# Optimization experiments

Hardware: AMD Instinct MI355X
Metric: run time of the kernel (lower is better)

## Reference

```python
import jax, jax.numpy as jnp
import numpy as np
import math

C = 512          # channels
K = 3            # conv kernel size
DILATIONS = (1, 3, 5)
RATIO = 2        # up/down sample ratio
FK = 12          # FIR anti-alias kernel size


def kaiser_sinc_filter1d(cutoff, half_width, kernel_size):
    # BigVGAN alias-free kaiser-windowed sinc lowpass filter
    half_size = kernel_size // 2
    delta_f = 4.0 * half_width
    A = 2.285 * (half_size - 1) * math.pi * delta_f + 7.95
    if A > 50.0:
        beta = 0.1102 * (A - 8.7)
    elif A >= 21.0:
        beta = 0.5842 * (A - 21.0) ** 0.4 + 0.07886 * (A - 21.0)
    else:
        beta = 0.0
    window = np.kaiser(kernel_size, beta)
    if kernel_size % 2 == 0:
        time = np.arange(-half_size, half_size) + 0.5
    else:
        time = np.arange(kernel_size) - half_size
    filt = 2.0 * cutoff * window * np.sinc(2.0 * cutoff * time)
    filt = filt / filt.sum()
    return jnp.asarray(filt, dtype=jnp.float32)

# Up/Down both use cutoff=0.5/ratio, half_width=0.6/ratio, kernel=12
AA_FILTER = kaiser_sinc_filter1d(0.5 / RATIO, 0.6 / RATIO, FK)

UP_PAD = FK // RATIO - 1                               # 5 (replicate pad before transpose conv)
UP_PAD_LEFT = UP_PAD * RATIO + (FK - RATIO) // 2       # 15
UP_PAD_RIGHT = UP_PAD * RATIO + (FK - RATIO + 1) // 2  # 15
DN_PAD_LEFT = FK // 2 - 1                              # 5 (even kernel)
DN_PAD_RIGHT = FK // 2                                 # 6


def _depthwise_conv(x, filt, stride=1, lhs_dilation=1, padding=(0, 0)):
    c = x.shape[1]
    w = jnp.broadcast_to(filt.reshape(1, 1, -1), (c, 1, filt.shape[0]))
    return jax.lax.conv_general_dilated(
        x, w, window_strides=(stride,), padding=[padding],
        lhs_dilation=(lhs_dilation,), dimension_numbers=('NCH', 'OIH', 'NCH'),
        feature_group_count=c)


def upsample2x(x):
    # replicate pad, depthwise transposed conv (lhs-dilated conv w/ flipped kernel), crop, scale
    x = jnp.pad(x, ((0, 0), (0, 0), (UP_PAD, UP_PAD)), mode='edge')
    y = RATIO * _depthwise_conv(x, AA_FILTER[::-1], lhs_dilation=RATIO,
                                padding=(FK - 1, FK - 1))
    return y[..., UP_PAD_LEFT:-UP_PAD_RIGHT]


def downsample2x(x):
    x = jnp.pad(x, ((0, 0), (0, 0), (DN_PAD_LEFT, DN_PAD_RIGHT)), mode='edge')
    return _depthwise_conv(x, AA_FILTER, stride=RATIO)


def snake_log(x, alpha, beta):
    # use_log_scale=True: alpha/beta are exponentiated; x + 1/(b+1e-5) * sin(a*x)^2
    a = jnp.exp(alpha)[None, :, None]
    b = jnp.exp(beta)[None, :, None]
    return x + (1.0 / (b + 1e-5)) * jnp.square(jnp.sin(x * a))


def aliasing_activation(x, alpha, beta):
    return downsample2x(snake_log(upsample2x(x), alpha, beta))


def weight_norm_conv1d(x, v, g, bias, dilation):
    # torch weight_norm dim=0: W[o] = g[o] * v[o] / ||v[o]||
    norm = jnp.sqrt(jnp.sum(v * v, axis=(1, 2), keepdims=True))
    w = g[:, None, None] * v / norm
    pad = (K * dilation - dilation) // 2
    y = jax.lax.conv_general_dilated(
        x, w, window_strides=(1,), padding=[(pad, pad)],
        rhs_dilation=(dilation,), dimension_numbers=('NCH', 'OIH', 'NCH'))
    return y + bias[None, :, None]


def setup_inputs() -> dict:
    key = jax.random.key(0)
    ks = jax.random.split(key, 12)
    B, T = 16, 4096
    return {
        'x': jax.random.normal(ks[0], (B, C, T), dtype=jnp.float32),
        'float_masks': jnp.ones((B, 1, T), dtype=jnp.float32),
        'in_snake_alpha': 0.1 * jax.random.normal(ks[1], (3, C), dtype=jnp.float32),
        'in_snake_beta': 0.1 * jax.random.normal(ks[2], (3, C), dtype=jnp.float32),
        'out_snake_alpha': 0.1 * jax.random.normal(ks[3], (3, C), dtype=jnp.float32),
        'out_snake_beta': 0.1 * jax.random.normal(ks[4], (3, C), dtype=jnp.float32),
        'in_conv_v': 0.05 * jax.random.normal(ks[5], (3, C, C, K), dtype=jnp.float32),
        'in_conv_g': 1.0 + 0.01 * jax.random.normal(ks[6], (3, C), dtype=jnp.float32),
        'in_conv_b': 0.01 * jax.random.normal(ks[7], (3, C), dtype=jnp.float32),
        'out_conv_v': 0.05 * jax.random.normal(ks[8], (3, C, C, K), dtype=jnp.float32),
        'out_conv_g': 1.0 + 0.01 * jax.random.normal(ks[9], (3, C), dtype=jnp.float32),
        'out_conv_b': 0.01 * jax.random.normal(ks[10], (3, C), dtype=jnp.float32),
    }


def reference(x, float_masks, in_snake_alpha, in_snake_beta, out_snake_alpha,
              out_snake_beta, in_conv_v, in_conv_g, in_conv_b, out_conv_v,
              out_conv_g, out_conv_b):
    for i, dilation in enumerate(DILATIONS):
        residuals = x
        x = aliasing_activation(x, in_snake_alpha[i], in_snake_beta[i]) * float_masks
        x = weight_norm_conv1d(x, in_conv_v[i], in_conv_g[i], in_conv_b[i], dilation)
        x = aliasing_activation(x, out_snake_alpha[i], out_snake_beta[i]) * float_masks
        x = weight_norm_conv1d(x, out_conv_v[i], out_conv_g[i], out_conv_b[i], 1)
        x = x + residuals
    return x * float_masks
```

## Files before the change

kernel.cpp:

```cpp
#include <hip/hip_runtime.h>
#include <cmath>

#define BN_ 16
#define CN_ 512
#define TN_ 4096
#define TPAD_ 4112
#define PADR_ 8

typedef float f32x4 __attribute__((ext_vector_type(4)));
typedef __bf16 bf16x8 __attribute__((ext_vector_type(8)));
typedef unsigned short u16x8 __attribute__((ext_vector_type(8)));

struct AAFilt { float g0[6]; float g1[6]; float fE[6]; float fO[6]; };

__device__ __forceinline__ unsigned short f2bf(float f) {
  unsigned u = __builtin_bit_cast(unsigned, f);
  u = (u + 0x7fffu + ((u >> 16) & 1u)) >> 16;
  return (unsigned short)u;
}
__device__ __forceinline__ float bf2f(unsigned short h) {
  return __builtin_bit_cast(float, (unsigned)h << 16);
}
__device__ __forceinline__ float to_f(float x) { return x; }
__device__ __forceinline__ float to_f(unsigned short x) { return bf2f(x); }

__device__ __forceinline__ void gld16(const void* g, void* l) {
  __builtin_amdgcn_global_load_lds((const __attribute__((address_space(1))) void*)g,
                                   (__attribute__((address_space(3))) void*)l,
                                   16, 0, 0);
}

__global__ __launch_bounds__(256) void prep_w(
    const float* __restrict__ vin, const float* __restrict__ gin,
    const float* __restrict__ vout, const float* __restrict__ gout,
    unsigned short* __restrict__ wpack)
{
  const int o = blockIdx.x;
  const int l = blockIdx.y;
  const int i = l >> 1, oc = l & 1;
  const float* v = (oc ? vout : vin) + (size_t)i * CN_ * CN_ * 3 + (size_t)o * CN_ * 3;
  const float g = (oc ? gout : gin)[i * CN_ + o];
  const int tid = threadIdx.x;

  float a = 0.f;
  for (int j = tid; j < 1536; j += 256) { float x = v[j]; a += x * x; }
  #pragma unroll
  for (int off = 32; off > 0; off >>= 1) a += __shfl_down(a, off);
  __shared__ float red[4];
  if ((tid & 63) == 0) red[tid >> 6] = a;
  __syncthreads();
  const float tot = red[0] + red[1] + red[2] + red[3];
  const float scale = g / sqrtf(tot);
  unsigned short* wl = wpack + (size_t)l * 3 * CN_ * CN_;
  for (int j = tid; j < 1536; j += 256) {
    int c = j / 3, k = j - 3 * c;
    wl[((size_t)k * CN_ + o) * CN_ + c] = f2bf(v[j] * scale);
  }
}

__global__ __launch_bounds__(256) void transpose_in(
    const float* __restrict__ src, float* __restrict__ dst)
{
  __shared__ float tile[32][33];
  const int b = blockIdx.z, c0 = blockIdx.y * 32, t0 = blockIdx.x * 32;
  const int tx = threadIdx.x & 31, ty = threadIdx.x >> 5;
  const float* s = src + ((size_t)b * CN_ + c0) * TN_ + t0;
  #pragma unroll
  for (int j = 0; j < 32; j += 8) tile[ty + j][tx] = s[(size_t)(ty + j) * TN_ + tx];
  __syncthreads();
  float* d = dst + ((size_t)b * TN_ + t0) * CN_ + c0;
  #pragma unroll
  for (int j = 0; j < 32; j += 8) d[(size_t)(ty + j) * CN_ + tx] = tile[tx][ty + j];
}

template <typename TIN>
__global__ __launch_bounds__(512) void act_kernel(
    const TIN* __restrict__ src, unsigned short* __restrict__ dst,
    const float* __restrict__ alpha, const float* __restrict__ beta,
    const float* __restrict__ mask, AAFilt F)
{
  const int c = threadIdx.x;
  const int b = blockIdx.y;
  const int seg = blockIdx.x;
  const int t0 = seg << 7;
  const float av = expf(alpha[c]);
  const float ib = 1.0f / (expf(beta[c]) + 1e-5f);
  const TIN* row = src + (size_t)b * TN_ * CN_ + c;
  unsigned short* drow = dst + (size_t)b * TPAD_ * CN_ + c;
  const float* mrow = mask + (size_t)b * TN_;

  if (seg == 0)  { for (int p = 0; p < PADR_; ++p) drow[(size_t)p * CN_] = 0; }
  if (seg == 31) { for (int p = 0; p < PADR_; ++p) drow[(size_t)(TPAD_ - PADR_ + p) * CN_] = 0; }

  auto ldx = [&](int t) -> float {
    t = t < 0 ? 0 : (t > TN_ - 1 ? TN_ - 1 : t);
    return to_f(row[(size_t)t * CN_]);
  };

  float xw[6];
  #pragma unroll
  for (int j = 0; j < 6; ++j) xw[j] = ldx(t0 - 5 + j);
  float sE[6], sO[6];
  #pragma unroll
  for (int j = 0; j < 6; ++j) { sE[j] = 0.f; sO[j] = 0.f; }
  float s_last = 0.f;

  auto step = [&](int tau, bool emit) {
    float uO = 0.f, uE = 0.f;
    #pragma unroll
    for (int j = 0; j < 6; ++j) { uO += F.g1[j] * xw[j]; uE += F.g0[j] * xw[j]; }
    float so = __sinf(uO * av); float sOn = uO + ib * so * so;
    float se = __sinf(uE * av); float sEn = uE + ib * se * se;
    if (tau + 2 == TN_ - 1) s_last = sOn;
    if (tau + 2 >= TN_) sOn = s_last;
    if (tau + 3 >= TN_) sEn = s_last;
    #pragma unroll
    for (int j = 0; j < 5; ++j) { sE[j] = sE[j + 1]; sO[j] = sO[j + 1]; }
    sE[5] = sEn; sO[5] = sOn;
    if (emit) {
      float d = 0.f;
      #pragma unroll
      for (int j = 0; j < 6; ++j) d += F.fE[j] * sE[j] + F.fO[j] * sO[j];
      d *= mrow[tau];
      drow[(size_t)(PADR_ + tau) * CN_] = f2bf(d);
    }
    #pragma unroll
    for (int j = 0; j < 5; ++j) xw[j] = xw[j + 1];
    xw[5] = ldx(tau + 6);
  };

  for (int w = 0; w < 5; ++w) step(t0 - 5 + w, false);
  if (t0 == 0) {
    float s0 = sE[3];
    sE[1] = s0; sE[2] = s0;
    sO[1] = s0; sO[2] = s0; sO[3] = s0;
  }
  for (int t = t0; t < t0 + 128; ++t) step(t, true);
}

#define ASZ (272 * 32)
#define BSZ (3 * 256 * 32)

template <int MODE>
__global__ __launch_bounds__(512, 2) void conv_kernel(
    const unsigned short* __restrict__ act,
    const unsigned short* __restrict__ wp,
    const float* __restrict__ bias,
    const float* __restrict__ res,
    const float* __restrict__ mask,
    void* __restrict__ outp, int dil)
{
  __shared__ __align__(16) unsigned short lA[2 * ASZ];
  __shared__ __align__(16) unsigned short lB[2 * BSZ];

  const int tid = threadIdx.x;
  const int bid = blockIdx.x;
  const int xcd = bid & 7, j = bid >> 3;
  const int ob = j & 1, tile = j >> 1;
  const int tt = tile * 8 + xcd;
  const int b = tt >> 4;
  const int t0 = (tt & 15) << 8;
  const int o0 = ob << 8;

  const int lane = tid & 63;
  const int wave = tid >> 6;
  const int wm = wave >> 2, wn = wave & 3;

  const f32x4 zero = {0.f, 0.f, 0.f, 0.f};
  f32x4 acc[8][4];
  #pragma unroll
  for (int a = 0; a < 8; ++a)
    #pragma unroll
    for (int n = 0; n < 4; ++n) acc[a][n] = zero;

  const unsigned short* aBase = act + ((size_t)b * TPAD_ + t0) * CN_;

  auto stage = [&](int bufi, int cb) {
    const int c0 = cb * 32;
    unsigned short* A = lA + (size_t)bufi * ASZ;
    unsigned short* B = lB + (size_t)bufi * BSZ;
    #pragma unroll
    for (int it = 0; it < 2; ++it) {
      int p = tid + it * 512;
      int r = p >> 2, pq = p & 3, gq = pq ^ (r & 3);
      gld16(aBase + (size_t)r * CN_ + c0 + gq * 8, A + (size_t)p * 8);
    }
    if (tid < 64) {
      int p = tid + 1024;
      int r = p >> 2, pq = p & 3, gq = pq ^ (r & 3);
      gld16(aBase + (size_t)r * CN_ + c0 + gq * 8, A + (size_t)p * 8);
    }
    #pragma unroll
    for (int it = 0; it < 6; ++it) {
      int p = tid + it * 512;
      int k = p >> 10, rem = p & 1023, ol = rem >> 2, pq = rem & 3;
      int gq = pq ^ (ol & 3);
      gld16(wp + ((size_t)(k * CN_ + o0 + ol)) * CN_ + c0 + gq * 8, B + (size_t)p * 8);
    }
  };

  stage(0, 0);
  __syncthreads();

  for (int cb = 0; cb < 16; ++cb) {
    const int cur = cb & 1;
    if (cb < 15) stage(cur ^ 1, cb + 1);
    const unsigned short* A = lA + (size_t)cur * ASZ;
    const unsigned short* B = lB + (size_t)cur * BSZ;

    #pragma unroll
    for (int k = 0; k < 3; ++k) {
      bf16x8 af[8], bfr[4];
      #pragma unroll
      for (int mi = 0; mi < 8; ++mi) {
        int r = wm * 128 + (lane & 15) + mi * 16 + PADR_ + (k - 1) * dil;
        int q = (lane >> 4) ^ (r & 3);
        af[mi] = __builtin_bit_cast(bf16x8, *reinterpret_cast<const u16x8*>(A + ((size_t)r * 4 + q) * 8));
      }
      #pragma unroll
      for (int ni = 0; ni < 4; ++ni) {
        int ol = wn * 64 + ni * 16 + (lane & 15);
        int q = (lane >> 4) ^ (ol & 3);
        bfr[ni] = __builtin_bit_cast(bf16x8, *reinterpret_cast<const u16x8*>(B + (((size_t)k * 256 + ol) * 4 + q) * 8));
      }
      __builtin_amdgcn_s_setprio(1);
      #pragma unroll
      for (int mi = 0; mi < 8; ++mi)
        #pragma unroll
        for (int ni = 0; ni < 4; ++ni)
          acc[mi][ni] = __builtin_amdgcn_mfma_f32_16x16x32_bf16(af[mi], bfr[ni], acc[mi][ni], 0, 0, 0);
      __builtin_amdgcn_s_setprio(0);
    }
    __syncthreads();
  }

  const int olane = lane & 15, rg = lane >> 4;
  const int obase = o0 + wn * 64 + olane;
  const int tbase = t0 + wm * 128 + rg * 4;

  if (MODE == 0) {
    unsigned short* O = (unsigned short*)outp + (size_t)b * TN_ * CN_;
    #pragma unroll
    for (int ni = 0; ni < 4; ++ni) {
      float bv = bias[obase + ni * 16];
      #pragma unroll
      for (int mi = 0; mi < 8; ++mi) {
        #pragma unroll
        for (int r = 0; r < 4; ++r) {
          int t = tbase + mi * 16 + r;
          O[(size_t)t * CN_ + obase + ni * 16] = f2bf(acc[mi][ni][r] + bv);
        }
      }
    }
  } else if (MODE == 1) {
    float* O = (float*)outp + (size_t)b * TN_ * CN_;
    const float* R = res + (size_t)b * TN_ * CN_;
    #pragma unroll
    for (int ni = 0; ni < 4; ++ni) {
      float bv = bias[obase + ni * 16];
      #pragma unroll
      for (int mi = 0; mi < 8; ++mi) {
        #pragma unroll
        for (int r = 0; r < 4; ++r) {
          int t = tbase + mi * 16 + r;
          size_t ix = (size_t)t * CN_ + obase + ni * 16;
          O[ix] = acc[mi][ni][r] + bv + R[ix];
        }
      }
    }
  } else {
    float* O = (float*)outp + (size_t)b * CN_ * TN_;
    const float* R = res + (size_t)b * TN_ * CN_;
    const float* M = mask + (size_t)b * TN_;
    float bv[4];
    #pragma unroll
    for (int ni = 0; ni < 4; ++ni) bv[ni] = bias[obase + ni * 16];
    #pragma unroll
    for (int mi = 0; mi < 8; ++mi) {
      int t = tbase + mi * 16;
      f32x4 mv = *reinterpret_cast<const f32x4*>(M + t);
      #pragma unroll
      for (int ni = 0; ni < 4; ++ni) {
        f32x4 v;
        #pragma unroll
        for (int r = 0; r < 4; ++r)
          v[r] = (acc[mi][ni][r] + bv[ni] + R[(size_t)(t + r) * CN_ + obase + ni * 16]) * mv[r];
        *reinterpret_cast<f32x4*>(O + (size_t)(obase + ni * 16) * TN_ + t) = v;
      }
    }
  }
}

static double bi0(double x) {
  double s = 1.0, t = 1.0, q = x * x * 0.25;
  for (int k = 1; k < 50; ++k) { t *= q / ((double)k * (double)k); s += t; if (t < 1e-18 * s) break; }
  return s;
}
static void make_filt(AAFilt* F) {
  const double PI = 3.14159265358979323846;
  double A = 2.285 * 5.0 * PI * 1.2 + 7.95;
  double beta;
  if (A > 50.0) beta = 0.1102 * (A - 8.7);
  else if (A >= 21.0) beta = 0.5842 * pow(A - 21.0, 0.4) + 0.07886 * (A - 21.0);
  else beta = 0.0;
  double i0b = bi0(beta);
  double f[12], sum = 0.0;
  for (int n = 0; n < 12; ++n) {
    double xx = 2.0 * n / 11.0 - 1.0;
    double w = bi0(beta * sqrt(fmax(0.0, 1.0 - xx * xx))) / i0b;
    double tt = (double)(n - 6) + 0.5;
    double arg = 0.5 * tt;
    double snc = sin(PI * arg) / (PI * arg);
    f[n] = 0.5 * w * snc;
    sum += f[n];
  }
  for (int n = 0; n < 12; ++n) f[n] /= sum;
  for (int j = 0; j < 6; ++j) {
    F->g0[j] = (float)(2.0 * f[11 - 2 * j]);
    F->g1[j] = (float)(2.0 * f[10 - 2 * j]);
    F->fE[j] = (float)f[2 * j + 1];
    F->fO[j] = (float)f[2 * j];
  }
}

extern "C" void kernel_launch(void* const* d_in, const int* in_sizes, int n_in,
                              void* d_out, int out_size, void* d_ws, size_t ws_size,
                              hipStream_t stream)
{
  (void)in_sizes; (void)n_in; (void)out_size; (void)ws_size;
  const float* x    = (const float*)d_in[0];
  const float* mask = (const float*)d_in[1];
  const float* inA  = (const float*)d_in[2];
  const float* inB  = (const float*)d_in[3];
  const float* outA = (const float*)d_in[4];
  const float* outB = (const float*)d_in[5];
  const float* vin  = (const float*)d_in[6];
  const float* gin  = (const float*)d_in[7];
  const float* bin  = (const float*)d_in[8];
  const float* vout = (const float*)d_in[9];
  const float* gout = (const float*)d_in[10];
  const float* bout = (const float*)d_in[11];

  char* ws = (char*)d_ws;
  float* xta           = (float*)ws;
  unsigned short* actb = (unsigned short*)(ws + 134217728);
  unsigned short* y1   = (unsigned short*)(ws + 134217728 + 67371008);
  unsigned short* wpk  = (unsigned short*)(ws + 134217728 + 67371008 + 67108864);

  AAFilt F; make_filt(&F);

  prep_w<<<dim3(512, 6), dim3(256), 0, stream>>>(vin, gin, vout, gout, wpk);
  transpose_in<<<dim3(128, 16, 16), dim3(256), 0, stream>>>(x, xta);

  const int dils[3] = {1, 3, 5};
  float* xcur = xta;
  float* dof = (float*)d_out;
  for (int i = 0; i < 3; ++i) {
    act_kernel<float><<<dim3(32, 16), dim3(512), 0, stream>>>(
        xcur, actb, inA + i * CN_, inB + i * CN_, mask, F);
    conv_kernel<0><<<dim3(512), dim3(512), 0, stream>>>(
        actb, wpk + (size_t)(2 * i) * 3 * CN_ * CN_, bin + i * CN_,
        nullptr, mask, (void*)y1, dils[i]);
    act_kernel<unsigned short><<<dim3(32, 16), dim3(512), 0, stream>>>(
        y1, actb, outA + i * CN_, outB + i * CN_, mask, F);
    if (i < 2) {
      float* xnext = (i == 0) ? dof : xta;
      conv_kernel<1><<<dim3(512), dim3(512), 0, stream>>>(
          actb, wpk + (size_t)(2 * i + 1) * 3 * CN_ * CN_, bout + i * CN_,
          xcur, mask, (void*)xnext, 1);
      xcur = xnext;
    } else {
      conv_kernel<2><<<dim3(512), dim3(512), 0, stream>>>(
          actb, wpk + (size_t)(2 * i + 1) * 3 * CN_ * CN_, bout + i * CN_,
          xcur, mask, d_out, 1);
    }
  }
}
```

Before: 1.253 ms.

## Interleave global prefetch with MFMA phases using fine-grained waitcnt and barriers

Restructures the conv GEMM main loop into six sub-phases per channel block. Each phase reads half of the A fragments plus the B fragments for one tap, issues part of the next block's global-to-LDS loads, and runs 16 MFMAs under raised priority. Explicit vmcnt and lgkmcnt waits replace whole-block __syncthreads, and the LDS swizzle changes from r&3 to (r>>1)&3. The goal is to overlap memory traffic with compute, reduce bank conflicts and cut register pressure from the A fragments. In exchange it adds many more barriers, and the hand-counted vmcnt values are fragile.

```diff
diff --git a/kernel.cpp b/kernel.cpp
--- a/kernel.cpp
+++ b/kernel.cpp
@@ -141,6 +141,43 @@
 #define ASZ (272 * 32)
 #define BSZ (3 * 256 * 32)
 
+#define VMCNT(n) asm volatile("s_waitcnt vmcnt(" #n ")" ::: "memory")
+#define LGKMCNT0 do { asm volatile("s_waitcnt lgkmcnt(0)" ::: "memory"); \
+                      __builtin_amdgcn_sched_barrier(0); } while (0)
+#define BAR __builtin_amdgcn_s_barrier()
+#define PRIO1 __builtin_amdgcn_s_setprio(1)
+#define PRIO0 __builtin_amdgcn_s_setprio(0)
+
+#define READ_A(k, mlo) do { \
+    const int rb_ = rbase[k] + (mlo) * 16; \
+    const int q_ = q4 ^ ((rb_ >> 1) & 3); \
+    const unsigned short* ap_ = A + ((size_t)rb_ * 4 + q_) * 8; \
+    af[0] = __builtin_bit_cast(bf16x8, *(const u16x8*)(ap_)); \
+    af[1] = __builtin_bit_cast(bf16x8, *(const u16x8*)(ap_ + 512)); \
+    af[2] = __builtin_bit_cast(bf16x8, *(const u16x8*)(ap_ + 1024)); \
+    af[3] = __builtin_bit_cast(bf16x8, *(const u16x8*)(ap_ + 1536)); \
+  } while (0)
+
+#define READ_B(k) do { \
+    const int ob_ = wn * 64 + l15; \
+    const int q_ = q4 ^ ((ob_ >> 1) & 3); \
+    const unsigned short* bp_ = Bc + (((size_t)(k) * 256 + ob_) * 4 + q_) * 8; \
+    bfr[0] = __builtin_bit_cast(bf16x8, *(const u16x8*)(bp_)); \
+    bfr[1] = __builtin_bit_cast(bf16x8, *(const u16x8*)(bp_ + 512)); \
+    bfr[2] = __builtin_bit_cast(bf16x8, *(const u16x8*)(bp_ + 1024)); \
+    bfr[3] = __builtin_bit_cast(bf16x8, *(const u16x8*)(bp_ + 1536)); \
+  } while (0)
+
+#define MFMA16(mlo) do { \
+    _Pragma("unroll") \
+    for (int mi_ = 0; mi_ < 4; ++mi_) { \
+      _Pragma("unroll") \
+      for (int ni_ = 0; ni_ < 4; ++ni_) \
+        acc[(mlo) + mi_][ni_] = __builtin_amdgcn_mfma_f32_16x16x32_bf16( \
+            af[mi_], bfr[ni_], acc[(mlo) + mi_][ni_], 0, 0, 0); \
+    } \
+  } while (0)
+
 template <int MODE>
 __global__ __launch_bounds__(512, 2) void conv_kernel(
     const unsigned short* __restrict__ act,
@@ -165,6 +202,7 @@
   const int lane = tid & 63;
   const int wave = tid >> 6;
   const int wm = wave >> 2, wn = wave & 3;
+  const int l15 = lane & 15, q4 = lane >> 4;
 
   const f32x4 zero = {0.f, 0.f, 0.f, 0.f};
   f32x4 acc[8][4];
@@ -175,68 +213,72 @@
 
   const unsigned short* aBase = act + ((size_t)b * TPAD_ + t0) * CN_;
 
-  auto stage = [&](int bufi, int cb) {
-    const int c0 = cb * 32;
-    unsigned short* A = lA + (size_t)bufi * ASZ;
-    unsigned short* B = lB + (size_t)bufi * BSZ;
-    #pragma unroll
-    for (int it = 0; it < 2; ++it) {
-      int p = tid + it * 512;
-      int r = p >> 2, pq = p & 3, gq = pq ^ (r & 3);
-      gld16(aBase + (size_t)r * CN_ + c0 + gq * 8, A + (size_t)p * 8);
-    }
+  int rbase[3];
+  #pragma unroll
+  for (int k = 0; k < 3; ++k) rbase[k] = wm * 128 + l15 + PADR_ + (k - 1) * dil;
+
+  auto stageA = [&](unsigned short* Ad, int c0) {
+    { int p = tid;       int r = p >> 2, pq = p & 3, gq = pq ^ ((r >> 1) & 3);
+      gld16(aBase + (size_t)r * CN_ + c0 + gq * 8, Ad + (size_t)p * 8); }
+    { int p = tid + 512; int r = p >> 2, pq = p & 3, gq = pq ^ ((r >> 1) & 3);
+      gld16(aBase + (size_t)r * CN_ + c0 + gq * 8, Ad + (size_t)p * 8); }
     if (tid < 64) {
-      int p = tid + 1024;
-      int r = p >> 2, pq = p & 3, gq = pq ^ (r & 3);
-      gld16(aBase + (size_t)r * CN_ + c0 + gq * 8, A + (size_t)p * 8);
-    }
-    #pragma unroll
-    for (int it = 0; it < 6; ++it) {
-      int p = tid + it * 512;
-      int k = p >> 10, rem = p & 1023, ol = rem >> 2, pq = rem & 3;
-      int gq = pq ^ (ol & 3);
-      gld16(wp + ((size_t)(k * CN_ + o0 + ol)) * CN_ + c0 + gq * 8, B + (size_t)p * 8);
-    }
+      int p = tid + 1024; int r = p >> 2, pq = p & 3, gq = pq ^ ((r >> 1) & 3);
+      gld16(aBase + (size_t)r * CN_ + c0 + gq * 8, Ad + (size_t)p * 8); }
   };
-
-  stage(0, 0);
-  __syncthreads();
-
-  for (int cb = 0; cb < 16; ++cb) {
-    const int cur = cb & 1;
-    if (cb < 15) stage(cur ^ 1, cb + 1);
-    const unsigned short* A = lA + (size_t)cur * ASZ;
-    const unsigned short* B = lB + (size_t)cur * BSZ;
-
-    #pragma unroll
-    for (int k = 0; k < 3; ++k) {
-      bf16x8 af[8], bfr[4];
-      #pragma unroll
-      for (int mi = 0; mi < 8; ++mi) {
-        int r = wm * 128 + (lane & 15) + mi * 16 + PADR_ + (k - 1) * dil;
-        int q = (lane >> 4) ^ (r & 3);
-        af[mi] = __builtin_bit_cast(bf16x8, *reinterpret_cast<const u16x8*>(A + ((size_t)r * 4 + q) * 8));
-      }
-      #pragma unroll
-      for (int ni = 0; ni < 4; ++ni) {
-        int ol = wn * 64 + ni * 16 + (lane & 15);
-        int q = (lane >> 4) ^ (ol & 3);
-        bfr[ni] = __builtin_bit_cast(bf16x8, *reinterpret_cast<const u16x8*>(B + (((size_t)k * 256 + ol) * 4 + q) * 8));
-      }
-      __builtin_amdgcn_s_setprio(1);
-      #pragma unroll
-      for (int mi = 0; mi < 8; ++mi)
-        #pragma unroll
-        for (int ni = 0; ni < 4; ++ni)
-          acc[mi][ni] = __builtin_amdgcn_mfma_f32_16x16x32_bf16(af[mi], bfr[ni], acc[mi][ni], 0, 0, 0);
-      __builtin_amdgcn_s_setprio(0);
-    }
-    __syncthreads();
-  }
-
-  const int olane = lane & 15, rg = lane >> 4;
-  const int obase = o0 + wn * 64 + olane;
-  const int tbase = t0 + wm * 128 + rg * 4;
+  auto stageB = [&](unsigned short* Bd, int c0, int k) {
+    { int p = tid;       int ol = p >> 2, pq = p & 3, gq = pq ^ ((ol >> 1) & 3);
+      gld16(wp + ((size_t)(k * CN_) + o0 + ol) * CN_ + c0 + gq * 8,
+            Bd + ((size_t)k * 1024 + p) * 8); }
+    { int p = tid + 512; int ol = p >> 2, pq = p & 3, gq = pq ^ ((ol >> 1) & 3);
+      gld16(wp + ((size_t)(k * CN_) + o0 + ol) * CN_ + c0 + gq * 8,
+            Bd + ((size_t)k * 1024 + p) * 8); }
+  };
+
+  stageA(lA, 0); stageB(lB, 0, 0); stageB(lB, 0, 1); stageB(lB, 0, 2);
+  VMCNT(4);
+  BAR;
+
+  for (int cb = 0; cb < 15; ++cb) {
+    const unsigned short* A  = lA + (size_t)(cb & 1) * ASZ;
+    const unsigned short* Bc = lB + (size_t)(cb & 1) * BSZ;
+    unsigned short* An = lA + (size_t)((cb & 1) ^ 1) * ASZ;
+    unsigned short* Bn = lB + (size_t)((cb & 1) ^ 1) * BSZ;
+    const int c0n = (cb + 1) * 32;
+    bf16x8 af[4], bfr[4];
+    READ_A(0, 0); READ_B(0); stageA(An, c0n);
+    BAR; LGKMCNT0; PRIO1; MFMA16(0); PRIO0; BAR;
+    READ_A(0, 4); stageB(Bn, c0n, 0);
+    BAR; LGKMCNT0; PRIO1; MFMA16(4); PRIO0; VMCNT(6); BAR;
+    READ_A(1, 0); READ_B(1); stageB(Bn, c0n, 1);
+    BAR; LGKMCNT0; PRIO1; MFMA16(0); PRIO0; BAR;
+    READ_A(1, 4); stageB(Bn, c0n, 2);
+    BAR; LGKMCNT0; PRIO1; MFMA16(4); PRIO0; VMCNT(6); BAR;
+    READ_A(2, 0); READ_B(2);
+    BAR; LGKMCNT0; PRIO1; MFMA16(0); PRIO0; BAR;
+    READ_A(2, 4);
+    BAR; LGKMCNT0; PRIO1; MFMA16(4); PRIO0; VMCNT(4); BAR;
+  }
+  {
+    const unsigned short* A  = lA + ASZ;
+    const unsigned short* Bc = lB + BSZ;
+    bf16x8 af[4], bfr[4];
+    READ_A(0, 0); READ_B(0);
+    BAR; LGKMCNT0; PRIO1; MFMA16(0); PRIO0; BAR;
+    READ_A(0, 4);
+    BAR; LGKMCNT0; PRIO1; MFMA16(4); PRIO0; VMCNT(2); BAR;
+    READ_A(1, 0); READ_B(1);
+    BAR; LGKMCNT0; PRIO1; MFMA16(0); PRIO0; BAR;
+    READ_A(1, 4);
+    BAR; LGKMCNT0; PRIO1; MFMA16(4); PRIO0; VMCNT(0); BAR;
+    READ_A(2, 0); READ_B(2);
+    BAR; LGKMCNT0; PRIO1; MFMA16(0); PRIO0; BAR;
+    READ_A(2, 4);
+    BAR; LGKMCNT0; PRIO1; MFMA16(4); PRIO0;
+  }
+
+  const int obase = o0 + wn * 64 + l15;
+  const int tbase = t0 + wm * 128 + q4 * 4;
 
   if (MODE == 0) {
     unsigned short* O = (unsigned short*)outp + (size_t)b * TN_ * CN_;
```

After: 1.187 ms. 5.3% less time.

## Loop output-channel halves per block, template dilation, and change LDS swizzle

Applied to the files above, without the earlier changes.

Each conv block now computes both 256-wide output-channel halves sequentially instead of launching separate blocks, halving the grid to 256 blocks. Dilation becomes a compile-time template parameter so row offsets fold into constants. The LDS XOR swizzle uses (row>>1)&3 to change the bank-conflict pattern, and s_setprio hints and the trailing barrier are removed. Halving the grid risks leaving compute units underused at two blocks per CU.

```diff
diff --git a/kernel.cpp b/kernel.cpp
--- a/kernel.cpp
+++ b/kernel.cpp
@@ -141,151 +141,153 @@
 #define ASZ (272 * 32)
 #define BSZ (3 * 256 * 32)
 
-template <int MODE>
+template <int MODE, int DIL>
 __global__ __launch_bounds__(512, 2) void conv_kernel(
     const unsigned short* __restrict__ act,
     const unsigned short* __restrict__ wp,
     const float* __restrict__ bias,
     const float* __restrict__ res,
     const float* __restrict__ mask,
-    void* __restrict__ outp, int dil)
+    void* __restrict__ outp)
 {
   __shared__ __align__(16) unsigned short lA[2 * ASZ];
   __shared__ __align__(16) unsigned short lB[2 * BSZ];
 
   const int tid = threadIdx.x;
   const int bid = blockIdx.x;
-  const int xcd = bid & 7, j = bid >> 3;
-  const int ob = j & 1, tile = j >> 1;
-  const int tt = tile * 8 + xcd;
+  const int xcd = bid & 7, grp = bid >> 3;
+  const int tt = grp * 8 + xcd;
   const int b = tt >> 4;
   const int t0 = (tt & 15) << 8;
-  const int o0 = ob << 8;
 
   const int lane = tid & 63;
   const int wave = tid >> 6;
   const int wm = wave >> 2, wn = wave & 3;
-
-  const f32x4 zero = {0.f, 0.f, 0.f, 0.f};
-  f32x4 acc[8][4];
-  #pragma unroll
-  for (int a = 0; a < 8; ++a)
-    #pragma unroll
-    for (int n = 0; n < 4; ++n) acc[a][n] = zero;
+  const int l15 = lane & 15, q4 = lane >> 4;
 
   const unsigned short* aBase = act + ((size_t)b * TPAD_ + t0) * CN_;
 
-  auto stage = [&](int bufi, int cb) {
+  auto stage = [&](int bufi, int cb, int o0) {
     const int c0 = cb * 32;
-    unsigned short* A = lA + (size_t)bufi * ASZ;
-    unsigned short* B = lB + (size_t)bufi * BSZ;
-    #pragma unroll
-    for (int it = 0; it < 2; ++it) {
-      int p = tid + it * 512;
-      int r = p >> 2, pq = p & 3, gq = pq ^ (r & 3);
-      gld16(aBase + (size_t)r * CN_ + c0 + gq * 8, A + (size_t)p * 8);
-    }
+    unsigned short* Ad = lA + (size_t)bufi * ASZ;
+    unsigned short* Bd = lB + (size_t)bufi * BSZ;
+    { int p = tid;       int r = p >> 2, pq = p & 3, gq = pq ^ ((r >> 1) & 3);
+      gld16(aBase + (size_t)r * CN_ + c0 + gq * 8, Ad + (size_t)p * 8); }
+    { int p = tid + 512; int r = p >> 2, pq = p & 3, gq = pq ^ ((r >> 1) & 3);
+      gld16(aBase + (size_t)r * CN_ + c0 + gq * 8, Ad + (size_t)p * 8); }
     if (tid < 64) {
       int p = tid + 1024;
-      int r = p >> 2, pq = p & 3, gq = pq ^ (r & 3);
-      gld16(aBase + (size_t)r * CN_ + c0 + gq * 8, A + (size_t)p * 8);
+      int r = p >> 2, pq = p & 3, gq = pq ^ ((r >> 1) & 3);
+      gld16(aBase + (size_t)r * CN_ + c0 + gq * 8, Ad + (size_t)p * 8);
     }
     #pragma unroll
     for (int it = 0; it < 6; ++it) {
       int p = tid + it * 512;
       int k = p >> 10, rem = p & 1023, ol = rem >> 2, pq = rem & 3;
-      int gq = pq ^ (ol & 3);
-      gld16(wp + ((size_t)(k * CN_ + o0 + ol)) * CN_ + c0 + gq * 8, B + (size_t)p * 8);
+      int gq = pq ^ ((ol >> 1) & 3);
+      gld16(wp + ((size_t)(k * CN_) + o0 + ol) * CN_ + c0 + gq * 8,
+            Bd + (size_t)p * 8);
     }
   };
 
-  stage(0, 0);
-  __syncthreads();
-
-  for (int cb = 0; cb < 16; ++cb) {
-    const int cur = cb & 1;
-    if (cb < 15) stage(cur ^ 1, cb + 1);
-    const unsigned short* A = lA + (size_t)cur * ASZ;
-    const unsigned short* B = lB + (size_t)cur * BSZ;
-
-    #pragma unroll
-    for (int k = 0; k < 3; ++k) {
-      bf16x8 af[8], bfr[4];
+  for (int h = 0; h < 2; ++h) {
+    const int o0 = h << 8;
+
+    const f32x4 zero = {0.f, 0.f, 0.f, 0.f};
+    f32x4 acc[8][4];
+    #pragma unroll
+    for (int a = 0; a < 8; ++a)
+      #pragma unroll
+      for (int n = 0; n < 4; ++n) acc[a][n] = zero;
+
+    stage(0, 0, o0);
+    __syncthreads();
+
+    for (int cb = 0; cb < 16; ++cb) {
+      const unsigned short* A  = lA + (size_t)(cb & 1) * ASZ;
+      const unsigned short* Bc = lB + (size_t)(cb & 1) * BSZ;
+      if (cb < 15) stage((cb & 1) ^ 1, cb + 1, o0);
+
+      #pragma unroll
+      for (int k = 0; k < 3; ++k) {
+        bf16x8 af[8], bfr[4];
+        const int rb0 = wm * 128 + l15 + PADR_ + (k - 1) * DIL;
+        #pragma unroll
+        for (int mi = 0; mi < 8; ++mi) {
+          int r = rb0 + mi * 16;
+          int q = q4 ^ ((r >> 1) & 3);
+          af[mi] = __builtin_bit_cast(bf16x8,
+                     *reinterpret_cast<const u16x8*>(A + ((size_t)r * 4 + q) * 8));
+        }
+        #pragma unroll
+        for (int ni = 0; ni < 4; ++ni) {
+          int ol = wn * 64 + ni * 16 + l15;
+          int q = q4 ^ ((ol >> 1) & 3);
+          bfr[ni] = __builtin_bit_cast(bf16x8,
+                      *reinterpret_cast<const u16x8*>(Bc + (((size_t)k * 256 + ol) * 4 + q) * 8));
+        }
+        #pragma unroll
+        for (int mi = 0; mi < 8; ++mi)
+          #pragma unroll
+          for (int ni = 0; ni < 4; ++ni)
+            acc[mi][ni] = __builtin_amdgcn_mfma_f32_16x16x32_bf16(
+                af[mi], bfr[ni], acc[mi][ni], 0, 0, 0);
+      }
+      if (cb < 15) __syncthreads();
+    }
+
+    const int obase = o0 + wn * 64 + l15;
+    const int tbase = t0 + wm * 128 + q4 * 4;
+
+    if (MODE == 0) {
+      unsigned short* O = (unsigned short*)outp + (size_t)b * TN_ * CN_;
+      #pragma unroll
+      for (int ni = 0; ni < 4; ++ni) {
+        float bv = bias[obase + ni * 16];
+        #pragma unroll
+        for (int mi = 0; mi < 8; ++mi) {
+          #pragma unroll
+          for (int r = 0; r < 4; ++r) {
+            int t = tbase + mi * 16 + r;
+            O[(size_t)t * CN_ + obase + ni * 16] = f2bf(acc[mi][ni][r] + bv);
+          }
+        }
+      }
+    } else if (MODE == 1) {
+      float* O = (float*)outp + (size_t)b * TN_ * CN_;
+      const float* R = res + (size_t)b * TN_ * CN_;
+      #pragma unroll
+      for (int ni = 0; ni < 4; ++ni) {
+        float bv = bias[obase + ni * 16];
+        #pragma unroll
+        for (int mi = 0; mi < 8; ++mi) {
+          #pragma unroll
+          for (int r = 0; r < 4; ++r) {
+            int t = tbase + mi * 16 + r;
+            size_t ix = (size_t)t * CN_ + obase + ni * 16;
+            O[ix] = acc[mi][ni][r] + bv + R[ix];
+          }
+        }
+      }
+    } else {
+      float* O = (float*)outp + (size_t)b * CN_ * TN_;
+      const float* R = res + (size_t)b * TN_ * CN_;
+      const float* M = mask + (size_t)b * TN_;
+      float bv[4];
+      #pragma unroll
+      for (int ni = 0; ni < 4; ++ni) bv[ni] = bias[obase + ni * 16];
       #pragma unroll
       for (int mi = 0; mi < 8; ++mi) {
-        int r = wm * 128 + (lane & 15) + mi * 16 + PADR_ + (k - 1) * dil;
-        int q = (lane >> 4) ^ (r & 3);
-        af[mi] = __builtin_bit_cast(bf16x8, *reinterpret_cast<const u16x8*>(A + ((size_t)r * 4 + q) * 8));
-      }
-      #pragma unroll
-      for (int ni = 0; ni < 4; ++ni) {
-        int ol = wn * 64 + ni * 16 + (lane & 15);
-        int q = (lane >> 4) ^ (ol & 3);
-        bfr[ni] = __builtin_bit_cast(bf16x8, *reinterpret_cast<const u16x8*>(B + (((size_t)k * 256 + ol) * 4 + q) * 8));
-      }
-      __builtin_amdgcn_s_setprio(1);
-      #pragma unroll
-      for (int mi = 0; mi < 8; ++mi)
-        #pragma unroll
-        for (int ni = 0; ni < 4; ++ni)
-          acc[mi][ni] = __builtin_amdgcn_mfma_f32_16x16x32_bf16(af[mi], bfr[ni], acc[mi][ni], 0, 0, 0);
-      __builtin_amdgcn_s_setprio(0);
-    }
-    __syncthreads();
-  }
-
-  const int olane = lane & 15, rg = lane >> 4;
-  const int obase = o0 + wn * 64 + olane;
-  const int tbase = t0 + wm * 128 + rg * 4;
-
-  if (MODE == 0) {
-    unsigned short* O = (unsigned short*)outp + (size_t)b * TN_ * CN_;
-    #pragma unroll
-    for (int ni = 0; ni < 4; ++ni) {
-      float bv = bias[obase + ni * 16];
-      #pragma unroll
-      for (int mi = 0; mi < 8; ++mi) {
-        #pragma unroll
-        for (int r = 0; r < 4; ++r) {
-          int t = tbase + mi * 16 + r;
-          O[(size_t)t * CN_ + obase + ni * 16] = f2bf(acc[mi][ni][r] + bv);
-        }
-      }
-    }
-  } else if (MODE == 1) {
-    float* O = (float*)outp + (size_t)b * TN_ * CN_;
-    const float* R = res + (size_t)b * TN_ * CN_;
-    #pragma unroll
-    for (int ni = 0; ni < 4; ++ni) {
-      float bv = bias[obase + ni * 16];
-      #pragma unroll
-      for (int mi = 0; mi < 8; ++mi) {
-        #pragma unroll
-        for (int r = 0; r < 4; ++r) {
-          int t = tbase + mi * 16 + r;
-          size_t ix = (size_t)t * CN_ + obase + ni * 16;
-          O[ix] = acc[mi][ni][r] + bv + R[ix];
-        }
-      }
-    }
-  } else {
-    float* O = (float*)outp + (size_t)b * CN_ * TN_;
-    const float* R = res + (size_t)b * TN_ * CN_;
-    const float* M = mask + (size_t)b * TN_;
-    float bv[4];
-    #pragma unroll
-    for (int ni = 0; ni < 4; ++ni) bv[ni] = bias[obase + ni * 16];
-    #pragma unroll
-    for (int mi = 0; mi < 8; ++mi) {
-      int t = tbase + mi * 16;
-      f32x4 mv = *reinterpret_cast<const f32x4*>(M + t);
-      #pragma unroll
-      for (int ni = 0; ni < 4; ++ni) {
-        f32x4 v;
-        #pragma unroll
-        for (int r = 0; r < 4; ++r)
-          v[r] = (acc[mi][ni][r] + bv[ni] + R[(size_t)(t + r) * CN_ + obase + ni * 16]) * mv[r];
-        *reinterpret_cast<f32x4*>(O + (size_t)(obase + ni * 16) * TN_ + t) = v;
+        int t = tbase + mi * 16;
+        f32x4 mv = *reinterpret_cast<const f32x4*>(M + t);
+        #pragma unroll
+        for (int ni = 0; ni < 4; ++ni) {
+          f32x4 v;
+          #pragma unroll
+          for (int r = 0; r < 4; ++r)
+            v[r] = (acc[mi][ni][r] + bv[ni] + R[(size_t)(t + r) * CN_ + obase + ni * 16]) * mv[r];
+          *reinterpret_cast<f32x4*>(O + (size_t)(obase + ni * 16) * TN_ + t) = v;
+        }
       }
     }
   }
@@ -352,27 +354,32 @@
   prep_w<<<dim3(512, 6), dim3(256), 0, stream>>>(vin, gin, vout, gout, wpk);
   transpose_in<<<dim3(128, 16, 16), dim3(256), 0, stream>>>(x, xta);
 
-  const int dils[3] = {1, 3, 5};
-  float* xcur = xta;
   float* dof = (float*)d_out;
-  for (int i = 0; i < 3; ++i) {
-    act_kernel<float><<<dim3(32, 16), dim3(512), 0, stream>>>(
-        xcur, actb, inA + i * CN_, inB + i * CN_, mask, F);
-    conv_kernel<0><<<dim3(512), dim3(512), 0, stream>>>(
-        actb, wpk + (size_t)(2 * i) * 3 * CN_ * CN_, bin + i * CN_,
-        nullptr, mask, (void*)y1, dils[i]);
-    act_kernel<unsigned short><<<dim3(32, 16), dim3(512), 0, stream>>>(
-        y1, actb, outA + i * CN_, outB + i * CN_, mask, F);
-    if (i < 2) {
-      float* xnext = (i == 0) ? dof : xta;
-      conv_kernel<1><<<dim3(512), dim3(512), 0, stream>>>(
-          actb, wpk + (size_t)(2 * i + 1) * 3 * CN_ * CN_, bout + i * CN_,
-          xcur, mask, (void*)xnext, 1);
-      xcur = xnext;
-    } else {
-      conv_kernel<2><<<dim3(512), dim3(512), 0, stream>>>(
-          actb, wpk + (size_t)(2 * i + 1) * 3 * CN_ * CN_, bout + i * CN_,
-          xcur, mask, d_out, 1);
-    }
-  }
-}
+
+  act_kernel<float><<<dim3(32, 16), dim3(512), 0, stream>>>(
+      xta, actb, inA + 0 * CN_, inB + 0 * CN_, mask, F);
+  conv_kernel<0, 1><<<dim3(256), dim3(512), 0, stream>>>(
+      actb, wpk + (size_t)0 * 3 * CN_ * CN_, bin + 0 * CN_, nullptr, mask, (void*)y1);
+  act_kernel<unsigned short><<<dim3(32, 16), dim3(512), 0, stream>>>(
+      y1, actb, outA + 0 * CN_, outB + 0 * CN_, mask, F);
+  conv_kernel<1, 1><<<dim3(256), dim3(512), 0, stream>>>(
+      actb, wpk + (size_t)1 * 3 * CN_ * CN_, bout + 0 * CN_, xta, mask, (void*)dof);
+
+  act_kernel<float><<<dim3(32, 16), dim3(512), 0, stream>>>(
+      dof, actb, inA + 1 * CN_, inB + 1 * CN_, mask, F);
+  conv_kernel<0, 3><<<dim3(256), dim3(512), 0, stream>>>(
+      actb, wpk + (size_t)2 * 3 * CN_ * CN_, bin + 1 * CN_, nullptr, mask, (void*)y1);
+  act_kernel<unsigned short><<<dim3(32, 16), dim3(512), 0, stream>>>(
+      y1, actb, outA + 1 * CN_, outB + 1 * CN_, mask, F);
+  conv_kernel<1, 1><<<dim3(256), dim3(512), 0, stream>>>(
+      actb, wpk + (size_t)3 * 3 * CN_ * CN_, bout + 1 * CN_, dof, mask, (void*)xta);
+
+  act_kernel<float><<<dim3(32, 16), dim3(512), 0, stream>>>(
+      xta, actb, inA + 2 * CN_, inB + 2 * CN_, mask, F);
+  conv_kernel<0, 5><<<dim3(256), dim3(512), 0, stream>>>(
+      actb, wpk + (size_t)4 * 3 * CN_ * CN_, bin + 2 * CN_, nullptr, mask, (void*)y1);
+  act_kernel<unsigned short><<<dim3(32, 16), dim3(512), 0, stream>>>(
+      y1, actb, outA + 2 * CN_, outB + 2 * CN_, mask, F);
+  conv_kernel<2, 1><<<dim3(256), dim3(512), 0, stream>>>(
+      actb, wpk + (size_t)5 * 3 * CN_ * CN_, bout + 2 * CN_, xta, mask, d_out);
+}
```

Result: slower. 1.576 ms (+25.7%).
